# Kernel tuning notes

Hardware: AMD Instinct MI355X
Metric: run time of the kernel (lower is better)

Reference implementation:

```python
import jax, jax.numpy as jnp
import numpy as np

BATCH = 262144
NUM_LAYERS = 64


def setup_inputs() -> dict:
    key = jax.random.key(0)
    k1, k2, k3 = jax.random.split(key, 3)
    X = jax.random.normal(k1, (BATCH, 2), dtype=jnp.float32)
    weights = jax.random.normal(k2, (NUM_LAYERS, 3), dtype=jnp.float32)
    biases = jax.random.normal(k3, (NUM_LAYERS, 3), dtype=jnp.float32)
    return {"X": X, "weights": weights, "biases": biases}


def _unitaries(X, weights, biases):
    # Pad data with constant 1 -> [B, 3]
    Xp = jnp.concatenate([X, jnp.ones((X.shape[0], 1), X.dtype)], axis=1)
    # angles[b, k, l] = weights[l, k] * Xp[b, k] + biases[l, k]  -> [B, 3, L]
    angles = Xp[:, :, None] * weights.T[None, :, :] + biases.T[None, :, :]
    phi, theta, omega = angles[:, 0, :], angles[:, 1, :], angles[:, 2, :]  # [B, L]
    ct = jnp.cos(theta / 2)
    st = jnp.sin(theta / 2)
    ppo = (phi + omega) / 2
    pmo = (phi - omega) / 2
    m00 = jnp.exp(-1j * ppo) * ct
    m01 = -jnp.exp(1j * pmo) * st
    m10 = jnp.exp(-1j * pmo) * st
    m11 = jnp.exp(1j * ppo) * ct
    # [B, L, 2, 2] -> [L, B, 2, 2]
    M = jnp.stack([jnp.stack([m00, m01], axis=-1),
                   jnp.stack([m10, m11], axis=-1)], axis=-2)
    return jnp.transpose(M, (1, 0, 2, 3))


def reference(X, weights, biases):
    M = _unitaries(X, weights, biases)  # [L, B, 2, 2] complex64
    B = X.shape[0]
    s0 = jnp.tile(jnp.array([1.0 + 0.0j, 0.0 + 0.0j], dtype=M.dtype), (B, 1))  # |0>

    def step(s, u):  # s: [B, 2], u: [B, 2, 2]
        s = jnp.einsum('bij,bj->bi', u, s)
        return s, s

    _, states = jax.lax.scan(step, s0, M)  # [L, B, 2] complex64
    return states
```

## Files before the change

kernel.cpp:

```cpp
#include <hip/hip_runtime.h>

#define BATCH 262144
#define NUM_LAYERS 64

typedef float f32x4 __attribute__((ext_vector_type(4)));

template <int MODE>
__global__ __launch_bounds__(256) void squbit_kernel(
    const float* __restrict__ X,
    const float* __restrict__ W,
    const float* __restrict__ Bi,
    float* __restrict__ out)
{
    __shared__ float4 cA[NUM_LAYERS];
    __shared__ float2 cOm[NUM_LAYERS];

    const int t = threadIdx.x;
    if (t < NUM_LAYERS) {
        const float w0 = W[t * 3 + 0], w1 = W[t * 3 + 1], w2 = W[t * 3 + 2];
        const float b0 = Bi[t * 3 + 0], b1 = Bi[t * 3 + 1], b2 = Bi[t * 3 + 2];
        float hom_prev = 0.0f;
        if (t > 0) hom_prev = 0.5f * (W[(t - 1) * 3 + 2] + Bi[(t - 1) * 3 + 2]);
        cA[t] = make_float4(0.5f * w0, fmaf(0.5f, b0, hom_prev), 0.5f * w1, 0.5f * b1);
        const float hom = 0.5f * (w2 + b2);
        float so, co;
        __sincosf(hom, &so, &co);
        cOm[t] = make_float2(co, so);
    }
    __syncthreads();

    const int g = blockIdx.x * 256 + t;
    const float4 xx = reinterpret_cast<const float4*>(X)[g];

    float Aur0 = 1.0f, Aui0 = 0.0f, Aur1 = 0.0f, Aui1 = 0.0f;
    float Bur0 = 1.0f, Bui0 = 0.0f, Bur1 = 0.0f, Bui1 = 0.0f;

    f32x4* o4 = reinterpret_cast<f32x4*>(out);

    #pragma unroll 8
    for (int l = 0; l < NUM_LAYERS; ++l) {
        const float4 c = cA[l];
        const float2 om = cOm[l];

        {
            const float hpsi = fmaf(xx.x, c.x, c.y);
            const float hth  = fmaf(xx.y, c.z, c.w);
            float sps, cps, sth, cth;
            __sincosf(hpsi, &sps, &cps);
            __sincosf(hth,  &sth, &cth);
            const float a0r = fmaf(Aui0,  sps, Aur0 * cps);
            const float a0i = fmaf(Aur0, -sps, Aui0 * cps);
            const float a1r = fmaf(Aui1, -sps, Aur1 * cps);
            const float a1i = fmaf(Aur1,  sps, Aui1 * cps);
            Aur0 = fmaf(-sth, a1r, cth * a0r);
            Aui0 = fmaf(-sth, a1i, cth * a0i);
            Aur1 = fmaf( sth, a0r, cth * a1r);
            Aui1 = fmaf( sth, a0i, cth * a1i);
        }
        {
            const float hpsi = fmaf(xx.z, c.x, c.y);
            const float hth  = fmaf(xx.w, c.z, c.w);
            float sps, cps, sth, cth;
            __sincosf(hpsi, &sps, &cps);
            __sincosf(hth,  &sth, &cth);
            const float a0r = fmaf(Bui0,  sps, Bur0 * cps);
            const float a0i = fmaf(Bur0, -sps, Bui0 * cps);
            const float a1r = fmaf(Bui1, -sps, Bur1 * cps);
            const float a1i = fmaf(Bur1,  sps, Bui1 * cps);
            Bur0 = fmaf(-sth, a1r, cth * a0r);
            Bui0 = fmaf(-sth, a1i, cth * a0i);
            Bur1 = fmaf( sth, a0r, cth * a1r);
            Bui1 = fmaf( sth, a0i, cth * a1i);
        }

        if (MODE == 0) {
            const float At0r = fmaf(Aui0,  om.y, Aur0 * om.x);
            const float At1r = fmaf(Aui1, -om.y, Aur1 * om.x);
            const float Bt0r = fmaf(Bui0,  om.y, Bur0 * om.x);
            const float Bt1r = fmaf(Bui1, -om.y, Bur1 * om.x);
            f32x4 v; v.x = At0r; v.y = At1r; v.z = Bt0r; v.w = Bt1r;
            __builtin_nontemporal_store(v, o4 + l * (BATCH / 2) + g);
        } else {
            const float At0r = fmaf(Aui0,  om.y, Aur0 * om.x);
            const float At0i = fmaf(Aur0, -om.y, Aui0 * om.x);
            const float At1r = fmaf(Aui1, -om.y, Aur1 * om.x);
            const float At1i = fmaf(Aur1,  om.y, Aui1 * om.x);
            const float Bt0r = fmaf(Bui0,  om.y, Bur0 * om.x);
            const float Bt0i = fmaf(Bur0, -om.y, Bui0 * om.x);
            const float Bt1r = fmaf(Bui1, -om.y, Bur1 * om.x);
            const float Bt1i = fmaf(Bur1,  om.y, Bui1 * om.x);
            f32x4 va; va.x = At0r; va.y = At0i; va.z = At1r; va.w = At1i;
            f32x4 vb; vb.x = Bt0r; vb.y = Bt0i; vb.z = Bt1r; vb.w = Bt1i;
            __builtin_nontemporal_store(va, o4 + (l * BATCH + 2 * g) + 0);
            __builtin_nontemporal_store(vb, o4 + (l * BATCH + 2 * g) + 1);
        }
    }
}

extern "C" void kernel_launch(void* const* d_in, const int* in_sizes, int n_in,
                              void* d_out, int out_size, void* d_ws, size_t ws_size,
                              hipStream_t stream) {
    const float* X  = (const float*)d_in[0];
    const float* W  = (const float*)d_in[1];
    const float* Bi = (const float*)d_in[2];
    float* out = (float*)d_out;

    dim3 grid(BATCH / 512), block(256);

    const long long full_complex_floats = (long long)NUM_LAYERS * BATCH * 4;
    if ((long long)out_size >= full_complex_floats) {
        squbit_kernel<1><<<grid, block, 0, stream>>>(X, W, Bi, out);
    } else {
        squbit_kernel<0><<<grid, block, 0, stream>>>(X, W, Bi, out);
    }
}
```

Before: 32.36 us.

## Split layer sequence into windows across blocks with prefix recompute

Each sample pair's 64-layer chain is split into 4 windows assigned to separate blocks, with each block recomputing the prefix of layers (without stores) to reach its window's start state. This raises the grid size fourfold to improve parallelism and occupancy. The cost is redundant compute, about 1.5x more sincos and rotation work overall. Nontemporal stores are also replaced with plain stores.

```diff
diff --git a/kernel.cpp b/kernel.cpp
--- a/kernel.cpp
+++ b/kernel.cpp
@@ -2,6 +2,8 @@
 
 #define BATCH 262144
 #define NUM_LAYERS 64
+#define WINDOWS 4
+#define WIN_LAYERS (NUM_LAYERS / WINDOWS)
 
 typedef float f32x4 __attribute__((ext_vector_type(4)));
 
@@ -29,7 +31,10 @@
     }
     __syncthreads();
 
-    const int g = blockIdx.x * 256 + t;
+    const int w  = blockIdx.x & (WINDOWS - 1);
+    const int g  = (blockIdx.x >> 2) * 256 + t;
+    const int l0 = w * WIN_LAYERS;
+
     const float4 xx = reinterpret_cast<const float4*>(X)[g];
 
     float Aur0 = 1.0f, Aui0 = 0.0f, Aur1 = 0.0f, Aui1 = 0.0f;
@@ -37,11 +42,45 @@
 
     f32x4* o4 = reinterpret_cast<f32x4*>(out);
 
-    #pragma unroll 8
-    for (int l = 0; l < NUM_LAYERS; ++l) {
+    #pragma unroll 4
+    for (int l = 0; l < l0; ++l) {
+        const float4 c = cA[l];
+        {
+            const float hpsi = fmaf(xx.x, c.x, c.y);
+            const float hth  = fmaf(xx.y, c.z, c.w);
+            float sps, cps, sth, cth;
+            __sincosf(hpsi, &sps, &cps);
+            __sincosf(hth,  &sth, &cth);
+            const float a0r = fmaf(Aui0,  sps, Aur0 * cps);
+            const float a0i = fmaf(Aur0, -sps, Aui0 * cps);
+            const float a1r = fmaf(Aui1, -sps, Aur1 * cps);
+            const float a1i = fmaf(Aur1,  sps, Aui1 * cps);
+            Aur0 = fmaf(-sth, a1r, cth * a0r);
+            Aui0 = fmaf(-sth, a1i, cth * a0i);
+            Aur1 = fmaf( sth, a0r, cth * a1r);
+            Aui1 = fmaf( sth, a0i, cth * a1i);
+        }
+        {
+            const float hpsi = fmaf(xx.z, c.x, c.y);
+            const float hth  = fmaf(xx.w, c.z, c.w);
+            float sps, cps, sth, cth;
+            __sincosf(hpsi, &sps, &cps);
+            __sincosf(hth,  &sth, &cth);
+            const float a0r = fmaf(Bui0,  sps, Bur0 * cps);
+            const float a0i = fmaf(Bur0, -sps, Bui0 * cps);
+            const float a1r = fmaf(Bui1, -sps, Bur1 * cps);
+            const float a1i = fmaf(Bur1,  sps, Bui1 * cps);
+            Bur0 = fmaf(-sth, a1r, cth * a0r);
+            Bui0 = fmaf(-sth, a1i, cth * a0i);
+            Bur1 = fmaf( sth, a0r, cth * a1r);
+            Bui1 = fmaf( sth, a0i, cth * a1i);
+        }
+    }
+
+    #pragma unroll 4
+    for (int l = l0; l < l0 + WIN_LAYERS; ++l) {
         const float4 c = cA[l];
         const float2 om = cOm[l];
-
         {
             const float hpsi = fmaf(xx.x, c.x, c.y);
             const float hth  = fmaf(xx.y, c.z, c.w);
@@ -79,7 +118,7 @@
             const float Bt0r = fmaf(Bui0,  om.y, Bur0 * om.x);
             const float Bt1r = fmaf(Bui1, -om.y, Bur1 * om.x);
             f32x4 v; v.x = At0r; v.y = At1r; v.z = Bt0r; v.w = Bt1r;
-            __builtin_nontemporal_store(v, o4 + l * (BATCH / 2) + g);
+            o4[l * (BATCH / 2) + g] = v;
         } else {
             const float At0r = fmaf(Aui0,  om.y, Aur0 * om.x);
             const float At0i = fmaf(Aur0, -om.y, Aui0 * om.x);
@@ -91,8 +130,8 @@
             const float Bt1i = fmaf(Bur1,  om.y, Bui1 * om.x);
             f32x4 va; va.x = At0r; va.y = At0i; va.z = At1r; va.w = At1i;
             f32x4 vb; vb.x = Bt0r; vb.y = Bt0i; vb.z = Bt1r; vb.w = Bt1i;
-            __builtin_nontemporal_store(va, o4 + (l * BATCH + 2 * g) + 0);
-            __builtin_nontemporal_store(vb, o4 + (l * BATCH + 2 * g) + 1);
+            o4[(l * BATCH + 2 * g) + 0] = va;
+            o4[(l * BATCH + 2 * g) + 1] = vb;
         }
     }
 }
@@ -105,7 +144,7 @@
     const float* Bi = (const float*)d_in[2];
     float* out = (float*)d_out;
 
-    dim3 grid(BATCH / 512), block(256);
+    dim3 grid((BATCH / 512) * WINDOWS), block(256);
 
     const long long full_complex_floats = (long long)NUM_LAYERS * BATCH * 4;
     if ((long long)out_size >= full_complex_floats) {
```

New measurement: 47.49 us. +46.7%, slower.
